# Optimization experiments

Measured on AMD Instinct MI355X. Metric: run time of the kernel, lower is better.

The kernel has to match this reference:

```python
import jax, jax.numpy as jnp
import numpy as np

B, DIM, H, W = 2, 192, 64, 64
HEADS = 4
EPS = 1e-12  # torch F.normalize eps


def conv2d(x, w, groups=1):
    # x: NCHW, w: OIHW, stride 1, SAME padding
    return jax.lax.conv_general_dilated(
        x, w, window_strides=(1, 1), padding='SAME',
        feature_group_count=groups,
        dimension_numbers=('NCHW', 'OIHW', 'NCHW'))


def setup_inputs() -> dict:
    key = jax.random.key(0)
    k1, k2, k3, k4 = jax.random.split(key, 4)
    x = jax.random.normal(k1, (B, DIM, H, W), dtype=jnp.float32)
    qkv_w = jax.random.normal(k2, (3 * DIM, DIM, 1, 1), dtype=jnp.float32) * 0.05
    dw_w = jax.random.normal(k3, (3 * DIM, 1, 3, 3), dtype=jnp.float32) * 0.05
    proj_w = jax.random.normal(k4, (DIM, DIM, 1, 1), dtype=jnp.float32) * 0.05
    temperature = jnp.ones((HEADS, 1, 1), dtype=jnp.float32)
    return {'x': x, 'qkv_w': qkv_w, 'dw_w': dw_w, 'proj_w': proj_w,
            'temperature': temperature}


def reference(x, qkv_w, dw_w, proj_w, temperature):
    b, dim, h, w = x.shape
    heads = temperature.shape[0]
    c = dim // heads  # per-head channels

    qkv = conv2d(conv2d(x, qkv_w), dw_w, groups=3 * dim)  # [b, 3*dim, h, w]
    q, k, v = jnp.split(qkv, 3, axis=1)

    def to_heads(t):
        # b (head c) h w -> b head (h w) c
        return t.reshape(b, heads, c, h * w).transpose(0, 1, 3, 2)

    q, k, v = to_heads(q), to_heads(k), to_heads(v)

    def l2norm(t):
        n = jnp.linalg.norm(t, axis=-1, keepdims=True)
        return t / jnp.maximum(n, EPS)

    q = l2norm(q)
    k = l2norm(k)

    # cosine attention with per-head learnable temperature
    attn = jnp.einsum('bnqc,bnkc->bnqk', q, k) * temperature[None]
    attn = jax.nn.softmax(attn, axis=-1)
    out = jnp.einsum('bnqk,bnkc->bnqc', attn, v)  # [b, head, hw, c]

    # b head (h w) c -> b (head c) h w
    out = out.transpose(0, 1, 3, 2).reshape(b, dim, h, w)
    return conv2d(out, proj_w)
```

## Files before the change

kernel.cpp:

```cpp
#include <hip/hip_runtime.h>
#include <cstdint>
#include <cstddef>

#define HW    4096
#define IMG   64
#define DIMC  192
#define NH    4
#define CH    48
#define CPAD  64
#define KVSPLIT 4
#define NTILE (HW / 64 / KVSPLIT)
#define LOG2E 1.4426950408889634f

typedef __bf16 bf16x8 __attribute__((ext_vector_type(8)));
typedef float  f32x4  __attribute__((ext_vector_type(4)));
typedef float  f32x16 __attribute__((ext_vector_type(16)));
typedef unsigned short u16x8 __attribute__((ext_vector_type(8)));
typedef unsigned int   u32x4 __attribute__((ext_vector_type(4)));

#if __has_builtin(__builtin_amdgcn_exp2f)
#define EXP2(x) __builtin_amdgcn_exp2f(x)
#else
#define EXP2(x) exp2f(x)
#endif

__device__ __forceinline__ unsigned short f2bf(float f) {
  unsigned int u = __builtin_bit_cast(unsigned int, f);
  u = (u + 0x7FFFu + ((u >> 16) & 1u)) >> 16;
  return (unsigned short)u;
}
__device__ __forceinline__ float bf2f(unsigned short u) {
  return __builtin_bit_cast(float, (unsigned int)u << 16);
}
__device__ __forceinline__ f32x4 mfma16(bf16x8 a, bf16x8 b, f32x4 c) {
  return __builtin_amdgcn_mfma_f32_16x16x32_bf16(a, b, c, 0, 0, 0);
}
__device__ __forceinline__ f32x16 mfma32(bf16x8 a, bf16x8 b, f32x16 c) {
  return __builtin_amdgcn_mfma_f32_32x32x16_bf16(a, b, c, 0, 0, 0);
}
__device__ __forceinline__ void gl16(const void* g, void* l) {
  __builtin_amdgcn_global_load_lds(
      (const __attribute__((address_space(1))) unsigned int*)g,
      (__attribute__((address_space(3))) unsigned int*)l, 16, 0, 0);
}
__device__ __forceinline__ unsigned int cvtpk(float lo, float hi) {
  unsigned int d;
  asm("v_cvt_pk_bf16_f32 %0, %1, %2" : "=v"(d) : "v"(lo), "v"(hi));
  return d;
}
__device__ __forceinline__ void swap32(unsigned int& a, unsigned int& b) {
  asm("v_permlane32_swap_b32 %0, %1" : "+v"(a), "+v"(b));
}

__global__ __launch_bounds__(256) void pack3_kernel(
    const float* __restrict__ x, const float* __restrict__ qkv_w,
    const float* __restrict__ proj_w, unsigned short* __restrict__ xb,
    unsigned short* __restrict__ wqkv, unsigned short* __restrict__ wproj) {
  const int bx = blockIdx.x, tid = threadIdx.x;
  if (bx < 128) {
    const int it = bx * 256 + tid;
    const int b = it >> 14;
    const int q4 = (it >> 12) & 3;
    const int p = it & 4095;
    const int c0 = q4 * 48;
    const float* src = x + ((size_t)b * DIMC + c0) * HW + p;
    float v[48];
    #pragma unroll
    for (int j = 0; j < 48; ++j) v[j] = src[(size_t)j * HW];
    #pragma unroll
    for (int g = 0; g < 6; ++g) {
      const int ch = c0 + g * 8;
      const int kc = ch >> 5, off = ch & 31;
      u16x8 gg;
      #pragma unroll
      for (int j = 0; j < 8; ++j) gg[j] = f2bf(v[g * 8 + j]);
      *(u16x8*)(xb + (((size_t)b * 6 + kc) * HW + p) * 32 + off) = gg;
    }
  } else {
    const int row = (bx - 128) * 256 + tid;
    if (row < 576) {
      const float* src = qkv_w + (size_t)row * DIMC;
      #pragma unroll
      for (int kc = 0; kc < 6; ++kc) {
        u16x8 g0, g1, g2, g3;
        #pragma unroll
        for (int j = 0; j < 8; ++j) {
          g0[j] = f2bf(src[kc * 32 + j]);      g1[j] = f2bf(src[kc * 32 + 8 + j]);
          g2[j] = f2bf(src[kc * 32 + 16 + j]); g3[j] = f2bf(src[kc * 32 + 24 + j]);
        }
        unsigned short* dst = wqkv + ((size_t)kc * 576 + row) * 32;
        *(u16x8*)dst = g0; *(u16x8*)(dst + 8) = g1;
        *(u16x8*)(dst + 16) = g2; *(u16x8*)(dst + 24) = g3;
      }
    } else {
      const int oc = row - 576;
      const float* src = proj_w + (size_t)oc * DIMC;
      #pragma unroll
      for (int kc = 0; kc < 6; ++kc) {
        u16x8 g0, g1, g2, g3;
        #pragma unroll
        for (int j = 0; j < 8; ++j) {
          g0[j] = f2bf(src[kc * 32 + j]);      g1[j] = f2bf(src[kc * 32 + 8 + j]);
          g2[j] = f2bf(src[kc * 32 + 16 + j]); g3[j] = f2bf(src[kc * 32 + 24 + j]);
        }
        unsigned short* dst = wproj + ((size_t)kc * DIMC + oc) * 32;
        *(u16x8*)dst = g0; *(u16x8*)(dst + 8) = g1;
        *(u16x8*)(dst + 16) = g2; *(u16x8*)(dst + 24) = g3;
      }
    }
  }
}

__global__ __launch_bounds__(256) void qkv_gemm_kernel(
    const unsigned short* __restrict__ xb, const unsigned short* __restrict__ wb,
    unsigned short* __restrict__ Cout) {
  const int tid = threadIdx.x;
  const int lane = tid & 63, wv = tid >> 6;
  const int l15 = lane & 15, l4 = lane >> 4;
  const int ocbase = blockIdx.x * 192;
  const int px0 = blockIdx.y * 64;
  const int b   = blockIdx.z;

  f32x4 acc[3][4];
  #pragma unroll
  for (int s = 0; s < 3; ++s)
    #pragma unroll
    for (int p = 0; p < 4; ++p) acc[s][p] = f32x4{0.f, 0.f, 0.f, 0.f};

  #pragma unroll
  for (int kc = 0; kc < 6; ++kc) {
    const unsigned short* xrow = xb + (((size_t)b * 6 + kc) * HW + px0 + l15) * 32 + l4 * 8;
    bf16x8 Bf[4];
    #pragma unroll
    for (int p = 0; p < 4; ++p) Bf[p] = *(const bf16x8*)(xrow + p * 512);
    #pragma unroll
    for (int s = 0; s < 3; ++s) {
      const int oc = ocbase + s * 64 + wv * 16 + l15;
      const bf16x8 af = *(const bf16x8*)(wb + ((size_t)kc * 576 + oc) * 32 + l4 * 8);
      #pragma unroll
      for (int p = 0; p < 4; ++p) acc[s][p] = mfma16(af, Bf[p], acc[s][p]);
    }
  }
  #pragma unroll
  for (int s = 0; s < 3; ++s) {
    unsigned short* Cb = Cout + ((size_t)b * 576 + ocbase + s * 64 + wv * 16) * HW + px0;
    #pragma unroll
    for (int p = 0; p < 4; ++p)
      #pragma unroll
      for (int r = 0; r < 4; ++r)
        Cb[(size_t)(l4 * 4 + r) * HW + p * 16 + l15] = f2bf(acc[s][p][r]);
  }
}

__global__ __launch_bounds__(256) void dw_conv3_kernel(
    const unsigned short* __restrict__ X, const float* __restrict__ W,
    unsigned short* __restrict__ Y) {
  __shared__ float T[66][72];
  const int bc = blockIdx.x;
  const int ch = bc % 576;
  const int tid = threadIdx.x;
  const unsigned short* Xb = X + (size_t)bc * HW;
  #pragma unroll
  for (int i = 0; i < 4; ++i) {
    const int idx = i * 256 + tid;
    const int row = idx >> 4, c4 = (idx & 15) << 2;
    const ushort4 u = *(const ushort4*)(Xb + row * 64 + c4);
    float4 f; f.x = bf2f(u.x); f.y = bf2f(u.y); f.z = bf2f(u.z); f.w = bf2f(u.w);
    *(float4*)&T[row + 1][c4 + 4] = f;
  }
  if (tid < 72) { T[0][tid] = 0.f; T[65][tid] = 0.f; }
  if (tid >= 128 && tid < 194) { const int r = tid - 128; T[r][3] = 0.f; T[r][68] = 0.f; }
  float w[9];
  #pragma unroll
  for (int i = 0; i < 9; ++i) w[i] = W[ch * 9 + i];
  __syncthreads();

  const int xx = tid & 63, ys = (tid >> 6) << 4;
  const int c = xx + 4;
  float a0 = T[ys][c - 1],     a1 = T[ys][c],     a2 = T[ys][c + 1];
  float b0 = T[ys + 1][c - 1], b1 = T[ys + 1][c], b2 = T[ys + 1][c + 1];
  unsigned short* Yb = Y + (size_t)bc * HW;
  #pragma unroll
  for (int k = 0; k < 16; ++k) {
    const float c0 = T[ys + k + 2][c - 1], c1 = T[ys + k + 2][c], c2 = T[ys + k + 2][c + 1];
    const float s = w[0] * a0 + w[1] * a1 + w[2] * a2
                  + w[3] * b0 + w[4] * b1 + w[5] * b2
                  + w[6] * c0 + w[7] * c1 + w[8] * c2;
    Yb[(ys + k) * 64 + xx] = f2bf(s);
    a0 = b0; a1 = b1; a2 = b2; b0 = c0; b1 = c1; b2 = c2;
  }
}

__global__ __launch_bounds__(256) void norm_pack3_kernel(
    const unsigned short* __restrict__ Dw, const float* __restrict__ temp,
    unsigned short* __restrict__ Qr, unsigned short* __restrict__ Kr,
    unsigned short* __restrict__ Vs) {
  const int px = blockIdx.x * 256 + threadIdx.x;
  const int sel = blockIdx.y >> 2, h = blockIdx.y & 3;
  const int b = blockIdx.z;
  const int bh = b * NH + h;
  const unsigned short* base = Dw + ((size_t)b * 576 + sel * DIMC + h * CH) * HW + px;

  float v[CH];
  if (sel == 2) {
    const int kt = px & ~63, kl = px & 63;
    #pragma unroll
    for (int c = 0; c < CH; ++c)
      Vs[((size_t)bh * CH + c) * HW + kt + (kl ^ ((c & 7) << 3))] = base[(size_t)c * HW];
    return;
  }
  float ss = 0.f;
  #pragma unroll
  for (int j = 0; j < CH; ++j) { v[j] = bf2f(base[(size_t)j * HW]); ss += v[j] * v[j]; }
  const u16x8 zz = {0, 0, 0, 0, 0, 0, 0, 0};
  if (sel == 0) {
    const float sc = temp[h] * LOG2E / fmaxf(sqrtf(ss), 1e-12f);
    u16x8 gr[8];
    #pragma unroll
    for (int g = 0; g < 6; ++g)
      #pragma unroll
      for (int j = 0; j < 8; ++j) gr[g][j] = f2bf(v[g * 8 + j] * sc);
    gr[6] = zz; gr[7] = zz;
    unsigned short* qrow = Qr + ((size_t)bh * HW + px) * CPAD;
    #pragma unroll
    for (int g = 0; g < 8; ++g) *(u16x8*)(qrow + g * 8) = gr[g];
  } else {
    const int ksw = (px & 3) | (((px >> 3) & 1) << 2);
    const float sc = 1.0f / fmaxf(sqrtf(ss), 1e-12f);
    u16x8 gr[8];
    #pragma unroll
    for (int g = 0; g < 6; ++g)
      #pragma unroll
      for (int j = 0; j < 8; ++j) gr[g][j] = f2bf(v[g * 8 + j] * sc);
    gr[6] = zz; gr[7] = zz;
    unsigned short* krow = Kr + ((size_t)bh * HW + px) * CPAD;
    #pragma unroll
    for (int g = 0; g < 8; ++g) *(u16x8*)(krow + (g ^ ksw) * 8) = gr[g];
  }
}

__global__ __launch_bounds__(256, 2) void flash8_kernel(
    const unsigned short* __restrict__ Qr,
    const unsigned short* __restrict__ Kr,
    const unsigned short* __restrict__ Vs,
    const float* __restrict__ temp,
    unsigned short* __restrict__ Opart, float* __restrict__ Lpart) {
  __shared__ __align__(16) union {
    struct { unsigned short Kl[2][4096]; unsigned short Vl[2][4096]; } s;
    float T[256][53];
  } lds;
  const int tid = threadIdx.x;
  const int lane = tid & 63, wv = tid >> 6;
  const int l31 = lane & 31, lhi = lane >> 5;
  const int bh = blockIdx.x, qt = blockIdx.y, sp = blockIdx.z;
  const int qb = qt * 256 + wv * 64;
  const float m = fabsf(temp[bh & 3]) * LOG2E * 1.05f + 0.1f;

  for (int i = tid; i < 1024; i += 256) {
    const unsigned short vv = (i < 64) ? (unsigned short)0x3F80 : (unsigned short)0;
    lds.s.Vl[0][3072 + i] = vv;
    lds.s.Vl[1][3072 + i] = vv;
  }

  const unsigned short* Qb = Qr + ((size_t)bh * HW + qb) * CPAD;
  bf16x8 qf[2][3];
  #pragma unroll
  for (int qb2 = 0; qb2 < 2; ++qb2)
    #pragma unroll
    for (int ci = 0; ci < 3; ++ci)
      qf[qb2][ci] = *(const bf16x8*)(Qb + (size_t)(qb2 * 32 + l31) * CPAD + ci * 16 + lhi * 8);

  const char* kg = (const char*)Kr + ((size_t)bh * HW + (size_t)sp * (HW / KVSPLIT)) * 128;
  const char* vg = (const char*)Vs + (size_t)bh * CH * HW * 2 + (size_t)sp * (HW / KVSPLIT) * 2;
  const int koA = tid * 16;
  const int vgA = (tid >> 3) * 8192 + (tid & 7) * 16;
  const int vgB = (32 + (tid >> 3)) * 8192 + (tid & 7) * 16;

  auto stage = [&](int buf, const char* kp, const char* vp) {
    char* kl = (char*)&lds.s.Kl[buf][0];
    gl16(kp + koA,        kl + koA);
    gl16(kp + 4096 + koA, kl + 4096 + koA);
    char* vl = (char*)&lds.s.Vl[buf][0];
    gl16(vp + vgA, vl + tid * 16);
    if (tid < 128) gl16(vp + vgB, vl + 4096 + tid * 16);
  };

  f32x16 o[2][2];
  #pragma unroll
  for (int cb = 0; cb < 2; ++cb)
    #pragma unroll
    for (int qb2 = 0; qb2 < 2; ++qb2)
      #pragma unroll
      for (int i = 0; i < 16; ++i) o[cb][qb2][i] = 0.f;
  f32x16 zin;
  #pragma unroll
  for (int i = 0; i < 16; ++i) zin[i] = -m;

  stage(0, kg, vg);
  kg += 8192; vg += 128;
  __syncthreads();
  int cur = 0;
  for (int t = 0; t < NTILE; ++t) {
    if (t + 1 < NTILE) { stage(cur ^ 1, kg, vg); kg += 8192; vg += 128; }
    const unsigned short* KL = &lds.s.Kl[cur][0];
    const unsigned short* VL = &lds.s.Vl[cur][0];

    f32x16 S[2][2];
    __builtin_amdgcn_s_setprio(1);
    #pragma unroll
    for (int kb = 0; kb < 2; ++kb) {
      const int krow = kb * 32 + l31;
      const int ksw = (krow & 3) | (((krow >> 3) & 1) << 2);
      bf16x8 kf[3];
      #pragma unroll
      for (int ci = 0; ci < 3; ++ci)
        kf[ci] = *(const bf16x8*)(KL + krow * 64 + (((ci * 2 + lhi) ^ ksw) * 8));
      #pragma unroll
      for (int qb2 = 0; qb2 < 2; ++qb2) {
        f32x16 acc = zin;
        #pragma unroll
        for (int ci = 0; ci < 3; ++ci) acc = mfma32(kf[ci], qf[qb2][ci], acc);
        S[kb][qb2] = acc;
      }
    }
    __builtin_amdgcn_s_setprio(0);

    #pragma unroll
    for (int kb = 0; kb < 2; ++kb) {
      #pragma unroll
      for (int qb2 = 0; qb2 < 2; ++qb2)
        #pragma unroll
        for (int i = 0; i < 16; ++i) S[kb][qb2][i] = EXP2(S[kb][qb2][i]);

      #pragma unroll
      for (int kh = 0; kh < 2; ++kh) {
        const int kc = kb * 2 + kh, rb = kh * 8;
        bf16x8 pb[2];
        #pragma unroll
        for (int qb2 = 0; qb2 < 2; ++qb2) {
          unsigned int w0 = cvtpk(S[kb][qb2][rb + 0], S[kb][qb2][rb + 1]);
          unsigned int w1 = cvtpk(S[kb][qb2][rb + 2], S[kb][qb2][rb + 3]);
          unsigned int w2 = cvtpk(S[kb][qb2][rb + 4], S[kb][qb2][rb + 5]);
          unsigned int w3 = cvtpk(S[kb][qb2][rb + 6], S[kb][qb2][rb + 7]);
          swap32(w0, w2);
          swap32(w1, w3);
          u32x4 ww = {w0, w1, w2, w3};
          pb[qb2] = __builtin_bit_cast(bf16x8, ww);
        }
        __builtin_amdgcn_s_setprio(1);
        #pragma unroll
        for (int cb = 0; cb < 2; ++cb) {
          const int crow = cb * 32 + l31;
          const bf16x8 vf = *(const bf16x8*)(VL + crow * 64 + (((kc * 2 + lhi) ^ (crow & 7)) * 8));
          #pragma unroll
          for (int qb2 = 0; qb2 < 2; ++qb2) o[cb][qb2] = mfma32(vf, pb[qb2], o[cb][qb2]);
        }
        __builtin_amdgcn_s_setprio(0);
      }
    }
    __syncthreads();
    cur ^= 1;
  }

  #pragma unroll
  for (int cb = 0; cb < 2; ++cb)
    #pragma unroll
    for (int qb2 = 0; qb2 < 2; ++qb2) {
      const int ql = wv * 64 + qb2 * 32 + l31;
      #pragma unroll
      for (int r = 0; r < 16; ++r) {
        const int c = cb * 32 + (r & 3) + 8 * (r >> 2) + 4 * lhi;
        if (c < 48) lds.T[ql][c] = o[cb][qb2][r];
      }
      if (lhi == 0) lds.T[ql][48] = o[1][qb2][8];
    }
  __syncthreads();
  {
    const int ql = tid;
    const int qg = qt * 256 + ql;
    float vv[48];
    #pragma unroll
    for (int c = 0; c < 48; ++c) vv[c] = lds.T[ql][c];
    const float Lv = lds.T[ql][48];
    unsigned short* Ob = Opart + ((size_t)(sp * 8 + bh) * HW + qg) * 48;
    #pragma unroll
    for (int g = 0; g < 6; ++g) {
      u16x8 gg;
      #pragma unroll
      for (int j = 0; j < 8; ++j) gg[j] = f2bf(vv[g * 8 + j]);
      *(u16x8*)(Ob + g * 8) = gg;
    }
    Lpart[(size_t)(sp * 8 + bh) * HW + qg] = Lv;
  }
}

__global__ __launch_bounds__(256) void proj_gemm2_kernel(
    const unsigned short* __restrict__ Opart, const float* __restrict__ Lpart,
    const unsigned short* __restrict__ wb, float* __restrict__ Cout) {
  __shared__ __align__(16) unsigned short BfL[384 * 8];
  const int tid = threadIdx.x;
  const int lane = tid & 63, wv = tid >> 6;
  const int l15 = lane & 15, l4 = lane >> 4;
  const int px0 = blockIdx.y * 16;
  const int b   = blockIdx.z;

  #pragma unroll
  for (int s0 = 0; s0 < 2; ++s0) {
    const int slot = s0 * 256 + tid;
    if (slot < 384) {
      const int kc = slot >> 6, q = slot & 63;
      const int sl4 = q >> 4, sl15 = q & 15;
      const int ch0 = kc * 32 + sl4 * 8;
      const int head = ch0 / 48, off = ch0 % 48;
      const int px = px0 + sl15;
      float ls = 0.f;
      #pragma unroll
      for (int sp = 0; sp < KVSPLIT; ++sp)
        ls += Lpart[(size_t)(sp * 8 + b * 4 + head) * HW + px];
      const float inv = 1.f / ls;
      float a8[8] = {};
      #pragma unroll
      for (int sp = 0; sp < KVSPLIT; ++sp) {
        const u16x8 u = *(const u16x8*)(Opart +
            ((size_t)(sp * 8 + b * 4 + head) * HW + px) * 48 + off);
        #pragma unroll
        for (int j = 0; j < 8; ++j) a8[j] += bf2f(u[j]);
      }
      u16x8 g;
      #pragma unroll
      for (int j = 0; j < 8; ++j) g[j] = f2bf(a8[j] * inv);
      *(u16x8*)&BfL[slot * 8] = g;
    }
  }
  __syncthreads();

  bf16x8 Bf[6];
  #pragma unroll
  for (int kc = 0; kc < 6; ++kc)
    Bf[kc] = *(const bf16x8*)&BfL[(kc * 64 + l4 * 16 + l15) * 8];

  #pragma unroll
  for (int s = 0; s < 3; ++s) {
    const int oc = s * 64 + wv * 16 + l15;
    f32x4 acc = {0.f, 0.f, 0.f, 0.f};
    #pragma unroll
    for (int kc = 0; kc < 6; ++kc) {
      const bf16x8 af = *(const bf16x8*)(wb + ((size_t)kc * DIMC + oc) * 32 + l4 * 8);
      acc = mfma16(af, Bf[kc], acc);
    }
    float* Cb = Cout + ((size_t)b * DIMC + s * 64 + wv * 16) * HW + px0;
    #pragma unroll
    for (int r = 0; r < 4; ++r)
      Cb[(size_t)(l4 * 4 + r) * HW + l15] = acc[r];
  }
}

extern "C" void kernel_launch(void* const* d_in, const int* in_sizes, int n_in,
                              void* d_out, int out_size, void* d_ws, size_t ws_size,
                              hipStream_t stream) {
  const float* x      = (const float*)d_in[0];
  const float* qkv_w  = (const float*)d_in[1];
  const float* dw_w   = (const float*)d_in[2];
  const float* proj_w = (const float*)d_in[3];
  const float* temp   = (const float*)d_in[4];

  char* ws = (char*)d_ws;
  unsigned short* xb    = (unsigned short*)(ws);
  unsigned short* wqkv  = (unsigned short*)(ws + 3145728);
  unsigned short* wproj = (unsigned short*)(ws + 3366912);
  unsigned short* qkvb  = (unsigned short*)(ws + 3440640);
  unsigned short* dwb   = (unsigned short*)(ws + 12877824);
  unsigned short* Qr    = (unsigned short*)(ws + 22315008);
  unsigned short* Kr    = (unsigned short*)(ws + 26509312);
  unsigned short* Vs    = (unsigned short*)(ws + 30703616);
  unsigned short* Opart = (unsigned short*)(ws + 33849344);
  float*          Lpart = (float*)(ws + 46432256);

  pack3_kernel<<<dim3(131), 256, 0, stream>>>(x, qkv_w, proj_w, xb, wqkv, wproj);
  qkv_gemm_kernel<<<dim3(3, 64, 2), 256, 0, stream>>>(xb, wqkv, qkvb);
  dw_conv3_kernel<<<dim3(1152), 256, 0, stream>>>(qkvb, dw_w, dwb);
  norm_pack3_kernel<<<dim3(16, 12, 2), 256, 0, stream>>>(dwb, temp, Qr, Kr, Vs);
  flash8_kernel<<<dim3(8, 16, KVSPLIT), 256, 0, stream>>>(Qr, Kr, Vs, temp, Opart, Lpart);
  proj_gemm2_kernel<<<dim3(1, 256, 2), 256, 0, stream>>>(Opart, Lpart, wproj, (float*)d_out);
}
```

Before: 78.55 us.

## Halve per-wave query tile in flash attention kernel to raise occupancy

Each wave now handles 32 query rows instead of 64, so a block covers 128 queries and the grid doubles along the query axis. Per-wave registers for Q fragments, score tiles and output accumulators are halved, and launch bounds now request 4 blocks per CU. The cost is that each K/V tile staged in LDS is reused by half as many queries, which doubles global K/V traffic and LDS reads per MFMA. Only half the threads take part in the epilogue store.

```diff
diff --git a/kernel.cpp b/kernel.cpp
--- a/kernel.cpp
+++ b/kernel.cpp
@@ -239,7 +239,7 @@
   }
 }
 
-__global__ __launch_bounds__(256, 2) void flash8_kernel(
+__global__ __launch_bounds__(256, 4) void flash10_kernel(
     const unsigned short* __restrict__ Qr,
     const unsigned short* __restrict__ Kr,
     const unsigned short* __restrict__ Vs,
@@ -247,13 +247,13 @@
     unsigned short* __restrict__ Opart, float* __restrict__ Lpart) {
   __shared__ __align__(16) union {
     struct { unsigned short Kl[2][4096]; unsigned short Vl[2][4096]; } s;
-    float T[256][53];
+    float T[128][53];
   } lds;
   const int tid = threadIdx.x;
   const int lane = tid & 63, wv = tid >> 6;
   const int l31 = lane & 31, lhi = lane >> 5;
   const int bh = blockIdx.x, qt = blockIdx.y, sp = blockIdx.z;
-  const int qb = qt * 256 + wv * 64;
+  const int qb = qt * 128 + wv * 32;
   const float m = fabsf(temp[bh & 3]) * LOG2E * 1.05f + 0.1f;
 
   for (int i = tid; i < 1024; i += 256) {
@@ -263,12 +263,10 @@
   }
 
   const unsigned short* Qb = Qr + ((size_t)bh * HW + qb) * CPAD;
-  bf16x8 qf[2][3];
-  #pragma unroll
-  for (int qb2 = 0; qb2 < 2; ++qb2)
-    #pragma unroll
-    for (int ci = 0; ci < 3; ++ci)
-      qf[qb2][ci] = *(const bf16x8*)(Qb + (size_t)(qb2 * 32 + l31) * CPAD + ci * 16 + lhi * 8);
+  bf16x8 qf[3];
+  #pragma unroll
+  for (int ci = 0; ci < 3; ++ci)
+    qf[ci] = *(const bf16x8*)(Qb + (size_t)l31 * CPAD + ci * 16 + lhi * 8);
 
   const char* kg = (const char*)Kr + ((size_t)bh * HW + (size_t)sp * (HW / KVSPLIT)) * 128;
   const char* vg = (const char*)Vs + (size_t)bh * CH * HW * 2 + (size_t)sp * (HW / KVSPLIT) * 2;
@@ -285,13 +283,11 @@
     if (tid < 128) gl16(vp + vgB, vl + 4096 + tid * 16);
   };
 
-  f32x16 o[2][2];
+  f32x16 o[2];
   #pragma unroll
   for (int cb = 0; cb < 2; ++cb)
     #pragma unroll
-    for (int qb2 = 0; qb2 < 2; ++qb2)
-      #pragma unroll
-      for (int i = 0; i < 16; ++i) o[cb][qb2][i] = 0.f;
+    for (int i = 0; i < 16; ++i) o[cb][i] = 0.f;
   f32x16 zin;
   #pragma unroll
   for (int i = 0; i < 16; ++i) zin[i] = -m;
@@ -305,55 +301,44 @@
     const unsigned short* KL = &lds.s.Kl[cur][0];
     const unsigned short* VL = &lds.s.Vl[cur][0];
 
-    f32x16 S[2][2];
+    f32x16 S[2];
     __builtin_amdgcn_s_setprio(1);
     #pragma unroll
     for (int kb = 0; kb < 2; ++kb) {
       const int krow = kb * 32 + l31;
       const int ksw = (krow & 3) | (((krow >> 3) & 1) << 2);
-      bf16x8 kf[3];
-      #pragma unroll
-      for (int ci = 0; ci < 3; ++ci)
-        kf[ci] = *(const bf16x8*)(KL + krow * 64 + (((ci * 2 + lhi) ^ ksw) * 8));
-      #pragma unroll
-      for (int qb2 = 0; qb2 < 2; ++qb2) {
-        f32x16 acc = zin;
-        #pragma unroll
-        for (int ci = 0; ci < 3; ++ci) acc = mfma32(kf[ci], qf[qb2][ci], acc);
-        S[kb][qb2] = acc;
+      f32x16 acc = zin;
+      #pragma unroll
+      for (int ci = 0; ci < 3; ++ci) {
+        const bf16x8 kf = *(const bf16x8*)(KL + krow * 64 + (((ci * 2 + lhi) ^ ksw) * 8));
+        acc = mfma32(kf, qf[ci], acc);
       }
+      S[kb] = acc;
     }
     __builtin_amdgcn_s_setprio(0);
 
     #pragma unroll
     for (int kb = 0; kb < 2; ++kb) {
       #pragma unroll
-      for (int qb2 = 0; qb2 < 2; ++qb2)
-        #pragma unroll
-        for (int i = 0; i < 16; ++i) S[kb][qb2][i] = EXP2(S[kb][qb2][i]);
+      for (int i = 0; i < 16; ++i) S[kb][i] = EXP2(S[kb][i]);
 
       #pragma unroll
       for (int kh = 0; kh < 2; ++kh) {
         const int kc = kb * 2 + kh, rb = kh * 8;
-        bf16x8 pb[2];
-        #pragma unroll
-        for (int qb2 = 0; qb2 < 2; ++qb2) {
-          unsigned int w0 = cvtpk(S[kb][qb2][rb + 0], S[kb][qb2][rb + 1]);
-          unsigned int w1 = cvtpk(S[kb][qb2][rb + 2], S[kb][qb2][rb + 3]);
-          unsigned int w2 = cvtpk(S[kb][qb2][rb + 4], S[kb][qb2][rb + 5]);
-          unsigned int w3 = cvtpk(S[kb][qb2][rb + 6], S[kb][qb2][rb + 7]);
-          swap32(w0, w2);
-          swap32(w1, w3);
-          u32x4 ww = {w0, w1, w2, w3};
-          pb[qb2] = __builtin_bit_cast(bf16x8, ww);
-        }
+        unsigned int w0 = cvtpk(S[kb][rb + 0], S[kb][rb + 1]);
+        unsigned int w1 = cvtpk(S[kb][rb + 2], S[kb][rb + 3]);
+        unsigned int w2 = cvtpk(S[kb][rb + 4], S[kb][rb + 5]);
+        unsigned int w3 = cvtpk(S[kb][rb + 6], S[kb][rb + 7]);
+        swap32(w0, w2);
+        swap32(w1, w3);
+        u32x4 ww = {w0, w1, w2, w3};
+        const bf16x8 pb = __builtin_bit_cast(bf16x8, ww);
         __builtin_amdgcn_s_setprio(1);
         #pragma unroll
         for (int cb = 0; cb < 2; ++cb) {
           const int crow = cb * 32 + l31;
           const bf16x8 vf = *(const bf16x8*)(VL + crow * 64 + (((kc * 2 + lhi) ^ (crow & 7)) * 8));
-          #pragma unroll
-          for (int qb2 = 0; qb2 < 2; ++qb2) o[cb][qb2] = mfma32(vf, pb[qb2], o[cb][qb2]);
+          o[cb] = mfma32(vf, pb, o[cb]);
         }
         __builtin_amdgcn_s_setprio(0);
       }
@@ -363,21 +348,19 @@
   }
 
   #pragma unroll
-  for (int cb = 0; cb < 2; ++cb)
-    #pragma unroll
-    for (int qb2 = 0; qb2 < 2; ++qb2) {
-      const int ql = wv * 64 + qb2 * 32 + l31;
-      #pragma unroll
-      for (int r = 0; r < 16; ++r) {
-        const int c = cb * 32 + (r & 3) + 8 * (r >> 2) + 4 * lhi;
-        if (c < 48) lds.T[ql][c] = o[cb][qb2][r];
-      }
-      if (lhi == 0) lds.T[ql][48] = o[1][qb2][8];
-    }
+  for (int cb = 0; cb < 2; ++cb) {
+    const int ql = wv * 32 + l31;
+    #pragma unroll
+    for (int r = 0; r < 16; ++r) {
+      const int c = cb * 32 + (r & 3) + 8 * (r >> 2) + 4 * lhi;
+      if (c < 48) lds.T[ql][c] = o[cb][r];
+    }
+    if (lhi == 0) lds.T[ql][48] = o[1][8];
+  }
   __syncthreads();
-  {
+  if (tid < 128) {
     const int ql = tid;
-    const int qg = qt * 256 + ql;
+    const int qg = qt * 128 + ql;
     float vv[48];
     #pragma unroll
     for (int c = 0; c < 48; ++c) vv[c] = lds.T[ql][c];
@@ -480,6 +463,6 @@
   qkv_gemm_kernel<<<dim3(3, 64, 2), 256, 0, stream>>>(xb, wqkv, qkvb);
   dw_conv3_kernel<<<dim3(1152), 256, 0, stream>>>(qkvb, dw_w, dwb);
   norm_pack3_kernel<<<dim3(16, 12, 2), 256, 0, stream>>>(dwb, temp, Qr, Kr, Vs);
-  flash8_kernel<<<dim3(8, 16, KVSPLIT), 256, 0, stream>>>(Qr, Kr, Vs, temp, Opart, Lpart);
+  flash10_kernel<<<dim3(8, 32, KVSPLIT), 256, 0, stream>>>(Qr, Kr, Vs, temp, Opart, Lpart);
   proj_gemm2_kernel<<<dim3(1, 256, 2), 256, 0, stream>>>(Opart, Lpart, wproj, (float*)d_out);
 }
```

After: 80.54 us. 1.03x slower.
